# Optimization experiments

Hardware: AMD Instinct MI355X
Metric: run time of the kernel (lower is better)

Reference implementation:

```python
import jax, jax.numpy as jnp
import numpy as np

N = 100000
E = 1600000
D_IN = 128
D_OUT = 128
EPS = 1e-5


def setup_inputs() -> dict:
    key = jax.random.key(0)
    ks = jax.random.split(key, 8)
    x = jax.random.normal(ks[0], (N, D_IN), dtype=jnp.float32)
    edge_index = jax.random.randint(ks[1], (2, E), 0, N, dtype=jnp.int64)
    s1 = 1.0 / np.sqrt(D_IN)
    s2 = 1.0 / np.sqrt(D_OUT)
    W1 = jax.random.uniform(ks[2], (D_IN, D_OUT), jnp.float32, -s1, s1)
    b1 = jax.random.uniform(ks[3], (D_OUT,), jnp.float32, -s1, s1)
    W2 = jax.random.uniform(ks[4], (D_OUT, D_OUT), jnp.float32, -s2, s2)
    b2 = jax.random.uniform(ks[5], (D_OUT,), jnp.float32, -s2, s2)
    gamma = jnp.ones((D_OUT,), jnp.float32)
    beta = jnp.zeros((D_OUT,), jnp.float32)
    return {"x": x, "edge_index": edge_index, "W1": W1, "b1": b1,
            "W2": W2, "b2": b2, "gamma": gamma, "beta": beta}


def reference(x, edge_index, W1, b1, W2, b2, gamma, beta):
    row, col = edge_index[0], edge_index[1]
    # scatter-add neighbor aggregation: agg[row] += x[col]
    agg = jax.ops.segment_sum(x[col], row, num_segments=N)
    h = x + agg  # residual (self) + aggregated neighbors
    # MLP: Linear -> ReLU -> Linear -> BatchNorm1d (training-mode batch stats)
    h = jax.nn.relu(h @ W1 + b1)
    h = h @ W2 + b2
    mean = jnp.mean(h, axis=0)
    var = jnp.mean(jnp.square(h - mean), axis=0)  # biased var, as torch BN uses
    out = gamma * (h - mean) * jax.lax.rsqrt(var + EPS) + beta
    return out
```

## Files before the change

### kernel.cpp

```cpp
#include <hip/hip_runtime.h>

#define N_NODES 100000
#define N_EDGES 1600000
#define DIM     128
#define EPS_BN  1e-5f
#define NB      512
#define NPB     196
#define NBLK    256
#define EPB     6250
#define CAP     4096
#define M_TILE  64
#define M_PAD   100032
#define GBLK    1563
#define LPITCH  136

typedef __attribute__((ext_vector_type(8))) short short8;
typedef __attribute__((ext_vector_type(4))) float floatx4;

__device__ __forceinline__ unsigned short f2bf(float f) {
    unsigned u = __float_as_uint(f);
    return (unsigned short)((u + 0x7FFF + ((u >> 16) & 1)) >> 16);
}
__device__ __forceinline__ float bf2f(unsigned short b) {
    return __uint_as_float((unsigned)b << 16);
}

__device__ __forceinline__ int detect64(const void* eidx) {
    int v = ((const int*)eidx)[2 * (threadIdx.x & 63) + 1];
    unsigned long long b = __ballot(v != 0);
    return (b == 0ULL) ? 1 : 0;
}
__device__ __forceinline__ int load_row(const void* eidx, int is64, int e) {
    if (is64) return (int)((const long long*)eidx)[e];
    return ((const int*)eidx)[e];
}
__device__ __forceinline__ int load_col(const void* eidx, int is64, int e) {
    if (is64) return (int)((const long long*)eidx)[N_EDGES + e];
    return ((const int*)eidx)[N_EDGES + e];
}

__global__ void convert_w(const float* __restrict__ W1,
                          const float* __restrict__ W2,
                          unsigned short* __restrict__ W1t,
                          unsigned short* __restrict__ W2t,
                          int* __restrict__ bcur, float* __restrict__ gstats) {
    if (blockIdx.x == 2) {
        int t = threadIdx.x;
        bcur[t] = 0;
        bcur[256 + t] = 0;
        if (t < 2 * DIM) gstats[t] = 0.f;
        return;
    }
    const float* W = blockIdx.x ? W2 : W1;
    unsigned short* Wt = blockIdx.x ? W2t : W1t;
    for (int i = threadIdx.x; i < DIM * DIM; i += 256) {
        int k = i >> 7, n = i & 127;
        Wt[n * DIM + k] = f2bf(W[i]);
    }
}

__global__ __launch_bounds__(1024) void bin_scatter_x(
    const void* eidx, int* bcur, unsigned* __restrict__ slots,
    const float* __restrict__ x, unsigned short* __restrict__ xb) {
    __shared__ int lh[NB];
    __shared__ int lbase[NB];
    __shared__ int loff[NB];
    __shared__ unsigned stage[EPB];
    __shared__ int gaddr[EPB];
    int t = threadIdx.x;
    int is64 = detect64(eidx);
    if (t < NB) lh[t] = 0;
    __syncthreads();
    int base = blockIdx.x * EPB;
    for (int i = t; i < EPB; i += 1024) {
        int r = load_row(eidx, is64, base + i);
        atomicAdd(&lh[r / NPB], 1);
    }
    __syncthreads();
    if (t < NB) loff[t] = lh[t];
    __syncthreads();
    for (int off = 1; off < NB; off <<= 1) {
        int a = (t >= off && t < NB) ? loff[t - off] : 0;
        __syncthreads();
        if (t < NB) loff[t] += a;
        __syncthreads();
    }
    if (t < NB) {
        int c = lh[t];
        lbase[t] = c ? atomicAdd(&bcur[t], c) : 0;
        loff[t] -= c;
        lh[t] = 0;
    }
    __syncthreads();
    for (int i = t; i < EPB; i += 1024) {
        int r = load_row(eidx, is64, base + i);
        int c = load_col(eidx, is64, base + i);
        int b = r / NPB;
        int pos = atomicAdd(&lh[b], 1);
        int idx = loff[b] + pos;
        stage[idx] = ((unsigned)(r - b * NPB) << 24) | (unsigned)c;
        gaddr[idx] = b * CAP + lbase[b] + pos;
    }
    __syncthreads();
    for (int i = t; i < EPB; i += 1024)
        slots[gaddr[i]] = stage[i];
    for (int i = blockIdx.x * 1024 + t; i < N_NODES * DIM / 4; i += NBLK * 1024) {
        float4 v = ((const float4*)x)[i];
        ushort4 o;
        o.x = f2bf(v.x); o.y = f2bf(v.y); o.z = f2bf(v.z); o.w = f2bf(v.w);
        ((ushort4*)xb)[i] = o;
    }
}

__global__ __launch_bounds__(1024) void build_csr(const unsigned* __restrict__ slots,
                                                  const int* __restrict__ bcnt,
                                                  int* __restrict__ rowst,
                                                  int* __restrict__ cols) {
    __shared__ int tmp[NB];
    __shared__ int hist[256];
    __shared__ int excl[256];
    __shared__ int cur[256];
    __shared__ int colbuf[CAP];
    int t = threadIdx.x;
    int b = blockIdx.x;
    if (t < NB) tmp[t] = bcnt[t];
    __syncthreads();
    for (int off = 1; off < NB; off <<= 1) {
        int a = (t >= off && t < NB) ? tmp[t - off] : 0;
        __syncthreads();
        if (t < NB) tmp[t] += a;
        __syncthreads();
    }
    int cnt = bcnt[b];
    int s = tmp[b] - cnt;
    int node0 = b * NPB;
    int nn = N_NODES - node0;
    if (nn > NPB) nn = NPB;
    const unsigned* pairs = slots + (size_t)b * CAP;
    if (t < 256) hist[t] = 0;
    if (b == NB - 1 && t == 0) rowst[N_NODES] = N_EDGES;
    __syncthreads();
    for (int i = t; i < cnt; i += 1024)
        atomicAdd(&hist[(int)(pairs[i] >> 24)], 1);
    __syncthreads();
    int v = (t < 256) ? hist[t] : 0;
    if (t < 256) excl[t] = v;
    __syncthreads();
    for (int off = 1; off < 256; off <<= 1) {
        int a = (t >= off && t < 256) ? excl[t - off] : 0;
        __syncthreads();
        if (t < 256) excl[t] += a;
        __syncthreads();
    }
    if (t < 256) {
        int ex = excl[t] - v;
        if (t < nn) rowst[node0 + t] = s + ex;
        cur[t] = ex;
    }
    __syncthreads();
    for (int i = t; i < cnt; i += 1024) {
        unsigned pr = pairs[i];
        int pos = atomicAdd(&cur[pr >> 24], 1);
        colbuf[pos] = (int)(pr & 0xFFFFFFu);
    }
    __syncthreads();
    for (int i = t; i < cnt; i += 1024) cols[s + i] = colbuf[i];
}

__global__ __launch_bounds__(256) void agg_kernel(
    const unsigned short* __restrict__ xb,
    const int* __restrict__ row_start, const int* __restrict__ cols,
    unsigned short* __restrict__ Hbf) {
    int wave = threadIdx.x >> 6;
    int lane = threadIdx.x & 63;
    int node = blockIdx.x * 4 + wave;
    const unsigned* xbw = (const unsigned*)xb;
    unsigned selfw = xbw[(size_t)node * 64 + lane];
    float2 acc;
    acc.x = __uint_as_float(selfw << 16);
    acc.y = __uint_as_float(selfw & 0xffff0000u);
    int s = row_start[node], e = row_start[node + 1];
    s = __builtin_amdgcn_readfirstlane(s);
    e = __builtin_amdgcn_readfirstlane(e);
    int d = e - s;
    if (d <= 16) {
        unsigned pw[16];
#pragma unroll
        for (int u = 0; u < 16; ++u) {
            int idx = s + u;
            int ci = (idx < e) ? idx : s;
            pw[u] = xbw[(size_t)cols[ci] * 64 + lane];
        }
#pragma unroll
        for (int u = 0; u < 16; ++u) {
            unsigned w = (u < d) ? pw[u] : 0u;
            acc.x += __uint_as_float(w << 16);
            acc.y += __uint_as_float(w & 0xffff0000u);
        }
    } else if (d <= 32) {
        unsigned pw[32];
#pragma unroll
        for (int u = 0; u < 32; ++u) {
            int idx = s + u;
            int ci = (idx < e) ? idx : s;
            pw[u] = xbw[(size_t)cols[ci] * 64 + lane];
        }
#pragma unroll
        for (int u = 0; u < 32; ++u) {
            unsigned w = (u < d) ? pw[u] : 0u;
            acc.x += __uint_as_float(w << 16);
            acc.y += __uint_as_float(w & 0xffff0000u);
        }
    } else {
        int j = s;
        for (; j + 16 <= e; j += 16) {
            unsigned pw[16];
#pragma unroll
            for (int u = 0; u < 16; ++u)
                pw[u] = xbw[(size_t)cols[j + u] * 64 + lane];
#pragma unroll
            for (int u = 0; u < 16; ++u) {
                acc.x += __uint_as_float(pw[u] << 16);
                acc.y += __uint_as_float(pw[u] & 0xffff0000u);
            }
        }
        for (; j < e; ++j) {
            unsigned pv = xbw[(size_t)cols[j] * 64 + lane];
            acc.x += __uint_as_float(pv << 16);
            acc.y += __uint_as_float(pv & 0xffff0000u);
        }
    }
    unsigned pack = (unsigned)f2bf(acc.x) | ((unsigned)f2bf(acc.y) << 16);
    ((unsigned*)Hbf)[(size_t)node * 64 + lane] = pack;
}

__global__ __launch_bounds__(256) void mlp_fused(
    const unsigned short* __restrict__ A,
    const unsigned short* __restrict__ B1t,
    const unsigned short* __restrict__ B2t,
    const float* __restrict__ bias1, const float* __restrict__ bias2,
    unsigned short* __restrict__ outb,
    float* __restrict__ gpart) {
    __shared__ unsigned short As[M_TILE * LPITCH];
    __shared__ unsigned short Bs[DIM * LPITCH];
    int t = threadIdx.x;
    int row0 = blockIdx.x * M_TILE;
    int lane = t & 63, wv = t >> 6;
    int m = lane & 15, g = lane >> 4;

#pragma unroll
    for (int i = 0; i < 4; ++i) {
        int ch = t + 256 * i;
        int r = ch >> 4, cc = ch & 15;
        *(uint4*)(&As[r * LPITCH + cc * 8]) =
            *(const uint4*)(&A[(size_t)(row0 + r) * DIM + cc * 8]);
    }
#pragma unroll
    for (int i = 0; i < 8; ++i) {
        int ch = t + 256 * i;
        int n = ch >> 4, cc = ch & 15;
        *(uint4*)(&Bs[n * LPITCH + cc * 8]) =
            *(const uint4*)(&B1t[n * DIM + cc * 8]);
    }
    __syncthreads();

    floatx4 acc1[8] = {};
#pragma unroll
    for (int kc = 0; kc < 4; ++kc) {
        short8 a = *(const short8*)(&As[(wv * 16 + m) * LPITCH + kc * 32 + g * 8]);
#pragma unroll
        for (int tt = 0; tt < 8; ++tt) {
            short8 b = *(const short8*)(&Bs[(tt * 16 + m) * LPITCH + kc * 32 + g * 8]);
            acc1[tt] = __builtin_amdgcn_mfma_f32_16x16x32_bf16(a, b, acc1[tt], 0, 0, 0);
        }
    }
    __syncthreads();

    uint4 wbuf[8];
#pragma unroll
    for (int i = 0; i < 8; ++i) {
        int ch = t + 256 * i;
        int n = ch >> 4, cc = ch & 15;
        wbuf[i] = *(const uint4*)(&B2t[n * DIM + cc * 8]);
    }
#pragma unroll
    for (int tt = 0; tt < 8; ++tt) {
        int col = tt * 16 + m;
        float bv = bias1[col];
#pragma unroll
        for (int j = 0; j < 4; ++j) {
            int rl = wv * 16 + g * 4 + j;
            As[rl * LPITCH + col] = f2bf(fmaxf(acc1[tt][j] + bv, 0.f));
        }
    }
#pragma unroll
    for (int i = 0; i < 8; ++i) {
        int ch = t + 256 * i;
        int n = ch >> 4, cc = ch & 15;
        *(uint4*)(&Bs[n * LPITCH + cc * 8]) = wbuf[i];
    }
    __syncthreads();

    floatx4 acc2[8] = {};
#pragma unroll
    for (int kc = 0; kc < 4; ++kc) {
        short8 a = *(const short8*)(&As[(wv * 16 + m) * LPITCH + kc * 32 + g * 8]);
#pragma unroll
        for (int tt = 0; tt < 8; ++tt) {
            short8 b = *(const short8*)(&Bs[(tt * 16 + m) * LPITCH + kc * 32 + g * 8]);
            acc2[tt] = __builtin_amdgcn_mfma_f32_16x16x32_bf16(a, b, acc2[tt], 0, 0, 0);
        }
    }

    float* csum = (float*)As;
    float* csq = csum + DIM;
    __syncthreads();
    if (t < DIM) { csum[t] = 0.f; csq[t] = 0.f; }
    __syncthreads();
#pragma unroll
    for (int tt = 0; tt < 8; ++tt) {
        int col = tt * 16 + m;
        float bv = bias2[col];
        float s = 0.f, q = 0.f;
#pragma unroll
        for (int j = 0; j < 4; ++j) {
            int row = row0 + wv * 16 + g * 4 + j;
            float v = acc2[tt][j] + bv;
            outb[(size_t)row * DIM + col] = f2bf(v);
            if (row < N_NODES) { s += v; q += v * v; }
        }
        atomicAdd(&csum[col], s);
        atomicAdd(&csq[col], q);
    }
    __syncthreads();
    gpart[(size_t)blockIdx.x * 256 + t] = (t < DIM) ? csum[t] : csq[t - DIM];
}

__global__ __launch_bounds__(256) void reduce_stats(
    const float* __restrict__ gpart, float* __restrict__ gstats) {
    int t = threadIdx.x;
    int chunk = (GBLK + 31) / 32;
    int r0 = blockIdx.x * chunk;
    int r1 = r0 + chunk < GBLK ? r0 + chunk : GBLK;
    float s = 0.f;
    for (int r = r0; r < r1; ++r) s += gpart[(size_t)r * 256 + t];
    atomicAdd(&gstats[t], s);
}

__global__ __launch_bounds__(256) void bn_apply(
    const unsigned short* __restrict__ H2, const float* __restrict__ gstats,
    const float* __restrict__ gamma, const float* __restrict__ beta,
    float* __restrict__ out) {
    __shared__ float sc_s[DIM], sh_s[DIM];
    int t = threadIdx.x;
    if (t < DIM) {
        float mean = gstats[t] * (1.0f / N_NODES);
        float m2 = gstats[DIM + t] * (1.0f / N_NODES);
        float var = m2 - mean * mean;
        float inv = rsqrtf(var + EPS_BN);
        float sc = gamma[t] * inv;
        sc_s[t] = sc;
        sh_s[t] = beta[t] - mean * sc;
    }
    __syncthreads();
    int i = blockIdx.x * 256 + t;
    int j4 = (i & 31) * 4;
    ushort4 hv = ((const ushort4*)H2)[i];
    float4 o;
    o.x = bf2f(hv.x) * sc_s[j4 + 0] + sh_s[j4 + 0];
    o.y = bf2f(hv.y) * sc_s[j4 + 1] + sh_s[j4 + 1];
    o.z = bf2f(hv.z) * sc_s[j4 + 2] + sh_s[j4 + 2];
    o.w = bf2f(hv.w) * sc_s[j4 + 3] + sh_s[j4 + 3];
    ((float4*)out)[i] = o;
}

extern "C" void kernel_launch(void* const* d_in, const int* in_sizes, int n_in,
                              void* d_out, int out_size, void* d_ws,
                              size_t ws_size, hipStream_t stream) {
    (void)in_sizes; (void)n_in; (void)out_size; (void)ws_size;
    const float* x     = (const float*)d_in[0];
    const void*  eidx  = d_in[1];
    const float* W1    = (const float*)d_in[2];
    const float* b1    = (const float*)d_in[3];
    const float* W2    = (const float*)d_in[4];
    const float* b2    = (const float*)d_in[5];
    const float* gamma = (const float*)d_in[6];
    const float* beta  = (const float*)d_in[7];
    float* out = (float*)d_out;

    char* p = (char*)d_ws;
    auto alloc = [&](size_t bytes) {
        char* r = p;
        p += (bytes + 255) & ~(size_t)255;
        return r;
    };
    unsigned short* Hbf  = (unsigned short*)alloc((size_t)M_PAD * DIM * 2);
    unsigned short* h2bf = (unsigned short*)alloc((size_t)M_PAD * DIM * 2);
    unsigned* slots = (unsigned*)h2bf;
    unsigned short* xb = (unsigned short*)alloc((size_t)N_NODES * DIM * 2);
    int*   cols   = (int*)alloc((size_t)(N_EDGES + 64) * 4);
    float* gpart  = (float*)alloc((size_t)GBLK * 256 * 4);
    int*   rowst  = (int*)alloc((size_t)(N_NODES + 1) * 4);
    int*   bcur   = (int*)alloc(NB * 4);
    unsigned short* W1t = (unsigned short*)alloc(DIM * DIM * 2);
    unsigned short* W2t = (unsigned short*)alloc(DIM * DIM * 2);
    float* gstats = (float*)alloc(2 * DIM * 4);

    convert_w<<<3, 256, 0, stream>>>(W1, W2, W1t, W2t, bcur, gstats);
    bin_scatter_x<<<NBLK, 1024, 0, stream>>>(eidx, bcur, slots, x, xb);
    build_csr<<<NB, 1024, 0, stream>>>(slots, bcur, rowst, cols);

    agg_kernel<<<N_NODES / 4, 256, 0, stream>>>(xb, rowst, cols, Hbf);

    mlp_fused<<<GBLK, 256, 0, stream>>>(Hbf, W1t, W2t, b1, b2, h2bf, gpart);
    reduce_stats<<<32, 256, 0, stream>>>(gpart, gstats);
    bn_apply<<<(N_NODES * DIM / 4) / 256, 256, 0, stream>>>(h2bf, gstats,
                                                            gamma, beta, out);
}
```

Baseline: 290.2 us.

## Fuse CSR build into aggregation, keeping per-bucket columns in LDS

Merges the build_csr and agg_kernel launches into one csr_agg kernel. Each block sorts its bucket's edges into shared memory and then gathers neighbour features straight from that LDS column list, so the global cols/rowst arrays and their write and read round trips go away. The cost is coarser parallelism: 512 blocks of 1024 threads, each handling about 196 nodes with 16 waves, instead of 25000 small blocks. It also adds clamps against bucket overflow (CAP) that silently drop edges if a bucket exceeds capacity.

```diff
diff --git a/kernel.cpp b/kernel.cpp
--- a/kernel.cpp
+++ b/kernel.cpp
@@ -98,8 +98,10 @@
         int b = r / NPB;
         int pos = atomicAdd(&lh[b], 1);
         int idx = loff[b] + pos;
+        int ga = lbase[b] + pos;
+        if (ga >= CAP) ga = CAP - 1;
         stage[idx] = ((unsigned)(r - b * NPB) << 24) | (unsigned)c;
-        gaddr[idx] = b * CAP + lbase[b] + pos;
+        gaddr[idx] = b * CAP + ga;
     }
     __syncthreads();
     for (int i = t; i < EPB; i += 1024)
@@ -112,126 +114,108 @@
     }
 }
 
-__global__ __launch_bounds__(1024) void build_csr(const unsigned* __restrict__ slots,
-                                                  const int* __restrict__ bcnt,
-                                                  int* __restrict__ rowst,
-                                                  int* __restrict__ cols) {
-    __shared__ int tmp[NB];
+__global__ __launch_bounds__(1024, 8) void csr_agg(
+    const unsigned short* __restrict__ xb,
+    const unsigned* __restrict__ slots,
+    const int* __restrict__ bcnt,
+    unsigned short* __restrict__ Hbf) {
     __shared__ int hist[256];
-    __shared__ int excl[256];
+    __shared__ int incl[256];
     __shared__ int cur[256];
     __shared__ int colbuf[CAP];
     int t = threadIdx.x;
     int b = blockIdx.x;
-    if (t < NB) tmp[t] = bcnt[t];
-    __syncthreads();
-    for (int off = 1; off < NB; off <<= 1) {
-        int a = (t >= off && t < NB) ? tmp[t - off] : 0;
-        __syncthreads();
-        if (t < NB) tmp[t] += a;
-        __syncthreads();
-    }
     int cnt = bcnt[b];
-    int s = tmp[b] - cnt;
+    if (cnt > CAP) cnt = CAP;
+    if (cnt < 0) cnt = 0;
     int node0 = b * NPB;
     int nn = N_NODES - node0;
     if (nn > NPB) nn = NPB;
+    if (nn < 0) nn = 0;
     const unsigned* pairs = slots + (size_t)b * CAP;
     if (t < 256) hist[t] = 0;
-    if (b == NB - 1 && t == 0) rowst[N_NODES] = N_EDGES;
     __syncthreads();
     for (int i = t; i < cnt; i += 1024)
         atomicAdd(&hist[(int)(pairs[i] >> 24)], 1);
     __syncthreads();
     int v = (t < 256) ? hist[t] : 0;
-    if (t < 256) excl[t] = v;
+    if (t < 256) incl[t] = v;
     __syncthreads();
     for (int off = 1; off < 256; off <<= 1) {
-        int a = (t >= off && t < 256) ? excl[t - off] : 0;
+        int a = (t >= off && t < 256) ? incl[t - off] : 0;
         __syncthreads();
-        if (t < 256) excl[t] += a;
+        if (t < 256) incl[t] += a;
         __syncthreads();
     }
-    if (t < 256) {
-        int ex = excl[t] - v;
-        if (t < nn) rowst[node0 + t] = s + ex;
-        cur[t] = ex;
-    }
+    if (t < 256) cur[t] = incl[t] - v;
     __syncthreads();
     for (int i = t; i < cnt; i += 1024) {
         unsigned pr = pairs[i];
         int pos = atomicAdd(&cur[pr >> 24], 1);
-        colbuf[pos] = (int)(pr & 0xFFFFFFu);
-    }
-    __syncthreads();
-    for (int i = t; i < cnt; i += 1024) cols[s + i] = colbuf[i];
-}
-
-__global__ __launch_bounds__(256) void agg_kernel(
-    const unsigned short* __restrict__ xb,
-    const int* __restrict__ row_start, const int* __restrict__ cols,
-    unsigned short* __restrict__ Hbf) {
-    int wave = threadIdx.x >> 6;
-    int lane = threadIdx.x & 63;
-    int node = blockIdx.x * 4 + wave;
+        if (pos < CAP) colbuf[pos] = (int)(pr & 0xFFFFFFu);
+    }
+    __syncthreads();
+
     const unsigned* xbw = (const unsigned*)xb;
-    unsigned selfw = xbw[(size_t)node * 64 + lane];
-    float2 acc;
-    acc.x = __uint_as_float(selfw << 16);
-    acc.y = __uint_as_float(selfw & 0xffff0000u);
-    int s = row_start[node], e = row_start[node + 1];
-    s = __builtin_amdgcn_readfirstlane(s);
-    e = __builtin_amdgcn_readfirstlane(e);
-    int d = e - s;
-    if (d <= 16) {
-        unsigned pw[16];
-#pragma unroll
-        for (int u = 0; u < 16; ++u) {
-            int idx = s + u;
-            int ci = (idx < e) ? idx : s;
-            pw[u] = xbw[(size_t)cols[ci] * 64 + lane];
-        }
-#pragma unroll
-        for (int u = 0; u < 16; ++u) {
-            unsigned w = (u < d) ? pw[u] : 0u;
-            acc.x += __uint_as_float(w << 16);
-            acc.y += __uint_as_float(w & 0xffff0000u);
-        }
-    } else if (d <= 32) {
-        unsigned pw[32];
-#pragma unroll
-        for (int u = 0; u < 32; ++u) {
-            int idx = s + u;
-            int ci = (idx < e) ? idx : s;
-            pw[u] = xbw[(size_t)cols[ci] * 64 + lane];
-        }
-#pragma unroll
-        for (int u = 0; u < 32; ++u) {
-            unsigned w = (u < d) ? pw[u] : 0u;
-            acc.x += __uint_as_float(w << 16);
-            acc.y += __uint_as_float(w & 0xffff0000u);
-        }
-    } else {
-        int j = s;
-        for (; j + 16 <= e; j += 16) {
+    int lane = t & 63, wv = t >> 6;
+    for (int nl = wv; nl < nn; nl += 16) {
+        int node = node0 + nl;
+        unsigned selfw = xbw[(size_t)node * 64 + lane];
+        float2 acc;
+        acc.x = __uint_as_float(selfw << 16);
+        acc.y = __uint_as_float(selfw & 0xffff0000u);
+        int e = incl[nl];
+        int s = nl ? incl[nl - 1] : 0;
+        s = __builtin_amdgcn_readfirstlane(s);
+        e = __builtin_amdgcn_readfirstlane(e);
+        int d = e - s;
+        if (d <= 16) {
             unsigned pw[16];
 #pragma unroll
-            for (int u = 0; u < 16; ++u)
-                pw[u] = xbw[(size_t)cols[j + u] * 64 + lane];
-#pragma unroll
             for (int u = 0; u < 16; ++u) {
-                acc.x += __uint_as_float(pw[u] << 16);
-                acc.y += __uint_as_float(pw[u] & 0xffff0000u);
+                int idx = s + u;
+                int ci = (idx < e) ? idx : s;
+                pw[u] = xbw[(size_t)colbuf[ci] * 64 + lane];
             }
-        }
-        for (; j < e; ++j) {
-            unsigned pv = xbw[(size_t)cols[j] * 64 + lane];
-            acc.x += __uint_as_float(pv << 16);
-            acc.y += __uint_as_float(pv & 0xffff0000u);
-        }
-    }
-    unsigned pack = (unsigned)f2bf(acc.x) | ((unsigned)f2bf(acc.y) << 16);
-    ((unsigned*)Hbf)[(size_t)node * 64 + lane] = pack;
+#pragma unroll
+            for (int u = 0; u < 16; ++u) {
+                unsigned w = (u < d) ? pw[u] : 0u;
+                acc.x += __uint_as_float(w << 16);
+                acc.y += __uint_as_float(w & 0xffff0000u);
+            }
+        } else {
+            int j = s;
+            for (; j + 16 <= e; j += 16) {
+                unsigned pw[16];
+#pragma unroll
+                for (int u = 0; u < 16; ++u)
+                    pw[u] = xbw[(size_t)colbuf[j + u] * 64 + lane];
+#pragma unroll
+                for (int u = 0; u < 16; ++u) {
+                    acc.x += __uint_as_float(pw[u] << 16);
+                    acc.y += __uint_as_float(pw[u] & 0xffff0000u);
+                }
+            }
+            if (j < e) {
+                unsigned pw[16];
+                int dd = e - j;
+#pragma unroll
+                for (int u = 0; u < 16; ++u) {
+                    int idx = j + u;
+                    int ci = (idx < e) ? idx : s;
+                    pw[u] = xbw[(size_t)colbuf[ci] * 64 + lane];
+                }
+#pragma unroll
+                for (int u = 0; u < 16; ++u) {
+                    unsigned w = (u < dd) ? pw[u] : 0u;
+                    acc.x += __uint_as_float(w << 16);
+                    acc.y += __uint_as_float(w & 0xffff0000u);
+                }
+            }
+        }
+        unsigned pack = (unsigned)f2bf(acc.x) | ((unsigned)f2bf(acc.y) << 16);
+        ((unsigned*)Hbf)[(size_t)node * 64 + lane] = pack;
+    }
 }
 
 __global__ __launch_bounds__(256) void mlp_fused(
@@ -398,9 +382,7 @@
     unsigned short* h2bf = (unsigned short*)alloc((size_t)M_PAD * DIM * 2);
     unsigned* slots = (unsigned*)h2bf;
     unsigned short* xb = (unsigned short*)alloc((size_t)N_NODES * DIM * 2);
-    int*   cols   = (int*)alloc((size_t)(N_EDGES + 64) * 4);
     float* gpart  = (float*)alloc((size_t)GBLK * 256 * 4);
-    int*   rowst  = (int*)alloc((size_t)(N_NODES + 1) * 4);
     int*   bcur   = (int*)alloc(NB * 4);
     unsigned short* W1t = (unsigned short*)alloc(DIM * DIM * 2);
     unsigned short* W2t = (unsigned short*)alloc(DIM * DIM * 2);
@@ -408,9 +390,7 @@
 
     convert_w<<<3, 256, 0, stream>>>(W1, W2, W1t, W2t, bcur, gstats);
     bin_scatter_x<<<NBLK, 1024, 0, stream>>>(eidx, bcur, slots, x, xb);
-    build_csr<<<NB, 1024, 0, stream>>>(slots, bcur, rowst, cols);
-
-    agg_kernel<<<N_NODES / 4, 256, 0, stream>>>(xb, rowst, cols, Hbf);
+    csr_agg<<<NB, 1024, 0, stream>>>(xb, slots, bcur, Hbf);
 
     mlp_fused<<<GBLK, 256, 0, stream>>>(Hbf, W1t, W2t, b1, b2, h2bf, gpart);
     reduce_stats<<<32, 256, 0, stream>>>(gpart, gstats);
```

Result: no change. 285.0 us (-1.8%).
